# Kernel tuning notes

Measured on AMD Instinct MI355X. Metric: run time of the kernel, lower is better.

Reference implementation:

```python
import jax, jax.numpy as jnp
import numpy as np

HRNN = 2e-11  # seconds per step; t grid is in nanoseconds (x1e9), step = 0.02
W0, W1 = -20.0, 10.0          # fixed oscillator coupling weights
X0 = (0.4736, 0.8745, 1.8497)  # fixed initial state


def setup_inputs() -> dict:
    key = jax.random.key(0)
    ks = jax.random.split(key, 9)
    B, T, NIN, NHI, NHO, NOUT = 1024, 2048, 8, 64, 64, 1
    g = lambda k, shape, s: jax.random.normal(k, shape, jnp.float32) * s
    return {
        "inputdata": jax.random.normal(ks[0], (B, T, NIN), jnp.float32),
        "Wni": g(ks[1], (NHI, NIN), 1.0 / np.sqrt(NIN)),   # nonlinearinput
        "bni": g(ks[2], (NHI,), 0.1),
        "Wli": g(ks[3], (1, NHI), 1.0 / np.sqrt(NHI)),     # linearinput
        "bli": g(ks[4], (1,), 0.1),
        "tau": jnp.zeros((1,), jnp.float32),                # nn.Parameter(Tensor(1))
        "Wn": g(ks[5], (NHO, 3), 1.0 / np.sqrt(3.0)),      # nonlinear readout
        "bn": g(ks[6], (NHO,), 0.1),
        "Wl": g(ks[7], (NOUT, NHO), 1.0 / np.sqrt(NHO)),   # linear readout
        "bl": g(ks[8], (NOUT,), 0.1),
    }


def reference(inputdata, Wni, bni, Wli, bli, tau, Wn, bn, Wl, bl):
    B, T, NIN = inputdata.shape
    tg = jnp.linspace(0.0, HRNN * (T - 1) * 1e9, T).astype(jnp.float32)
    u = inputdata  # [B, T, NIN]
    x0 = jnp.broadcast_to(jnp.array(X0, jnp.float32)[None, :], (B, 3))

    def lin_interp(t):
        # clamp-to-edge linear interpolation of u along the time grid
        ind = jnp.clip(jnp.searchsorted(tg, t), 1, T - 1)
        t_lo, t_hi = tg[ind - 1], tg[ind]
        frac = jnp.clip((t - t_lo) / (t_hi - t_lo), 0.0, 1.0)
        u_lo = u[:, ind - 1, :]
        return u_lo + (u[:, ind, :] - u_lo) * frac  # [B, NIN]

    def f(t, x):
        ut = lin_interp(t)
        dparam = jax.nn.sigmoid(ut @ Wni.T + bni) @ Wli.T + bli  # [B, 1]
        tx = jnp.tanh(x)
        dx = jnp.stack(
            (-x[:, 0] + tx[:, 1],
             -x[:, 1] + tx[:, 2],
             -x[:, 2] + W0 * tx[:, 0] + W1 * tx[:, 1]),
            axis=1,
        )
        return dx / jnp.exp(tau + dparam)  # [B, 3]

    def step(x, ts):
        # torchdiffeq 'rk4' = fourth-order 3/8 rule between grid points
        t0, t1 = ts
        h = t1 - t0
        k1 = f(t0, x)
        k2 = f(t0 + h / 3, x + h * k1 / 3)
        k3 = f(t0 + 2 * h / 3, x + h * (k2 - k1 / 3))
        k4 = f(t1, x + h * (k1 - k2 + k3))
        xn = x + h * (k1 + 3 * k2 + 3 * k3 + k4) / 8
        return xn, xn

    _, xs = jax.lax.scan(step, x0, (tg[:-1], tg[1:]))  # [T-1, B, 3]
    outrnn = jnp.concatenate([x0[None], xs], axis=0).transpose(1, 0, 2)  # [B, T, 3]
    hid = jax.nn.sigmoid(outrnn @ Wn.T + bn)  # [B, T, NHO]
    return hid @ Wl.T + bl  # [B, T, NOUT]
```

## Files before the change

kernel.cpp:

```cpp
#include <hip/hip_runtime.h>

#define BB 1024
#define TT 2048
#define NIN 8
#define NHI 64

#define CS 2.8853900817779268f
#define NL2E 1.4426950408889634f
#define DELTA (40.94f / 2047.0f)

typedef float v2f __attribute__((ext_vector_type(2)));

__device__ __forceinline__ v2f vfma(v2f a, v2f b, v2f c) {
    return __builtin_elementwise_fma(a, b, c);
}

template<int CTRL>
__device__ __forceinline__ float qperm(float x) {
    int r = __builtin_amdgcn_mov_dpp(__float_as_int(x), CTRL, 0xF, 0xF, true);
    return __int_as_float(r);
}

__global__ __launch_bounds__(256) void precompute_r(
    const float* __restrict__ u, const float* __restrict__ Wni,
    const float* __restrict__ bni, const float* __restrict__ Wli,
    const float* __restrict__ bli, const float* __restrict__ tau,
    float* __restrict__ r3)
{
    int lt = threadIdx.x;
    int lane = lt & 63;
    int gw = blockIdx.x * 4 + (lt >> 6);
    int b = gw / 33;
    int chunk = gw % 33;
    int s = chunk * 63 + lane;
    int sc = s < TT ? s : TT - 1;
    int b2 = b + 512;

    const float4* upA = reinterpret_cast<const float4*>(u + ((long long)b  * TT + sc) * NIN);
    const float4* upB = reinterpret_cast<const float4*>(u + ((long long)b2 * TT + sc) * NIN);
    float4 A0 = upA[0], A1 = upA[1];
    float4 B0 = upB[0], B1 = upB[1];
    v2f u0 = {A0.x, B0.x}, u1 = {A0.y, B0.y}, u2 = {A0.z, B0.z}, u3 = {A0.w, B0.w};
    v2f u4 = {A1.x, B1.x}, u5 = {A1.y, B1.y}, u6 = {A1.z, B1.z}, u7 = {A1.w, B1.w};

    v2f d0 = {0.f, 0.f}, d1 = {0.f, 0.f}, d2 = {0.f, 0.f};
    #pragma unroll 8
    for (int j = 0; j < NHI; j++) {
        const float* wj = Wni + j * NIN;
        float bj = bni[j];
        v2f z = {bj, bj};
        z = vfma((v2f){wj[0], wj[0]}, u0, z);
        z = vfma((v2f){wj[1], wj[1]}, u1, z);
        z = vfma((v2f){wj[2], wj[2]}, u2, z);
        z = vfma((v2f){wj[3], wj[3]}, u3, z);
        z = vfma((v2f){wj[4], wj[4]}, u4, z);
        z = vfma((v2f){wj[5], wj[5]}, u5, z);
        z = vfma((v2f){wj[6], wj[6]}, u6, z);
        z = vfma((v2f){wj[7], wj[7]}, u7, z);
        v2f zn;
        zn.x = __shfl_down(z.x, 1);
        zn.y = __shfl_down(z.y, 1);
        v2f dz = zn - z;
        v2f zc  = z  * (v2f){-NL2E, -NL2E};
        v2f dzc = dz * (v2f){-NL2E / 3.0f, -NL2E / 3.0f};
        v2f e0, edz;
        e0.x  = __builtin_amdgcn_exp2f(zc.x);
        e0.y  = __builtin_amdgcn_exp2f(zc.y);
        edz.x = __builtin_amdgcn_exp2f(dzc.x);
        edz.y = __builtin_amdgcn_exp2f(dzc.y);
        v2f e1 = e0 * edz;
        v2f e2 = e1 * edz;
        v2f q0 = e0 + 1.0f, q1 = e1 + 1.0f, q2 = e2 + 1.0f;
        v2f P12 = q1 * q2;
        v2f Dn = q0 * P12;
        v2f rD;
        rD.x = __builtin_amdgcn_rcpf(Dn.x);
        rD.y = __builtin_amdgcn_rcpf(Dn.y);
        v2f P02 = q0 * q2;
        v2f P01 = q0 * q1;
        float wl = Wli[j];
        v2f wr = rD * (v2f){wl, wl};
        d0 = vfma(wr, P12, d0);
        d1 = vfma(wr, P02, d1);
        d2 = vfma(wr, P01, d2);
    }
    float base = tau[0] + bli[0];
    float g0a = DELTA * __builtin_amdgcn_exp2f((base + d0.x) * -NL2E);
    float g1a = DELTA * __builtin_amdgcn_exp2f((base + d1.x) * -NL2E);
    float g2a = DELTA * __builtin_amdgcn_exp2f((base + d2.x) * -NL2E);
    float g0b = DELTA * __builtin_amdgcn_exp2f((base + d0.y) * -NL2E);
    float g1b = DELTA * __builtin_amdgcn_exp2f((base + d1.y) * -NL2E);
    float g2b = DELTA * __builtin_amdgcn_exp2f((base + d2.y) * -NL2E);

    if (s < TT) {
        float* pA = r3 + ((long long)b  * TT + s) * 3;
        float* pB = r3 + ((long long)b2 * TT + s) * 3;
        pA[0] = g0a;
        pB[0] = g0b;
        if (lane < 63 && s < TT - 1) {
            pA[1] = g1a; pA[2] = g2a;
            pB[1] = g1b; pB[2] = g2b;
        }
    }
}

__global__ __launch_bounds__(64) void scan_kernel(
    const float* __restrict__ r3, float* __restrict__ xs)
{
    int gt = blockIdx.x * 64 + threadIdx.x;
    int b = gt >> 2;
    int l = gt & 3;

    const float4* rp = reinterpret_cast<const float4*>(r3 + (long long)b * TT * 3);
    int comp = (l == 3) ? 1 : l;
    float* xc = xs + (long long)comp * BB * TT + (long long)b * TT;

    bool is2 = (l == 2);
    float cA = is2 ? 40.0f * CS : -2.0f * CS;
    float cB = is2 ? -20.0f * CS : 0.0f;
    float Kl = is2 ? -10.0f * CS : CS;

    float X = (l == 0) ? 0.4736f * CS : (is2 ? 1.8497f * CS : 0.8745f * CS);

#define STEP(G1v, G2v, G3v, G4v) do { \
    float g1 = (G1v), g2 = (G2v), g3 = (G3v); \
    float q  = g1 * (1.0f / 3.0f); \
    float g4_8 = (G4v) * 0.125f; \
    float cA1 = q * cA,    cB1 = q * cB; \
    float cA2 = g2 * cA,   cB2 = g2 * cB; \
    float cA3 = g3 * cA,   cB3 = g3 * cB; \
    float cA4 = g4_8 * cA, cB4 = g4_8 * cB; \
     \
    float e1 = __builtin_amdgcn_exp2f(X); \
    float rho1 = __builtin_amdgcn_rcpf(1.0f + e1); \
    float KmX = Kl - X; \
    float pb2 = fmaf(q, KmX, X); \
    float p11 = qperm<0x89>(rho1), p21 = qperm<0x10>(rho1); \
    float S2 = fmaf(cA1, p11, fmaf(cB1, p21, pb2)); \
    float V1 = fmaf(cA, p11, cB * p21); \
    float W1 = V1 + KmX; \
     \
    float e2 = __builtin_amdgcn_exp2f(S2); \
    float rho2 = __builtin_amdgcn_rcpf(1.0f + e2); \
    float KmS2 = Kl - S2; \
    float pb3 = fmaf(g2, KmS2, fmaf(-q, W1, X)); \
    float p12 = qperm<0x89>(rho2), p22 = qperm<0x10>(rho2); \
    float S3 = fmaf(cA2, p12, fmaf(cB2, p22, pb3)); \
    float V2 = fmaf(cA, p12, cB * p22); \
    float W2 = V2 + KmS2; \
     \
    float e3 = __builtin_amdgcn_exp2f(S3); \
    float rho3 = __builtin_amdgcn_rcpf(1.0f + e3); \
    float KmS3 = Kl - S3; \
    float pb4 = fmaf(g3, KmS3, fmaf(-g2, W2, fmaf(g1, W1, X))); \
    float p13 = qperm<0x89>(rho3), p23 = qperm<0x10>(rho3); \
    float S4 = fmaf(cA3, p13, fmaf(cB3, p23, pb4)); \
    float V3 = fmaf(cA, p13, cB * p23); \
    float W3 = V3 + KmS3; \
     \
    float e4 = __builtin_amdgcn_exp2f(S4); \
    float rho4 = __builtin_amdgcn_rcpf(1.0f + e4); \
    float KmS4 = Kl - S4; \
    float t3 = fmaf(3.0f * g3, W3, fmaf(3.0f * g2, W2, g1 * W1)); \
    float pbX = fmaf(g4_8, KmS4, fmaf(0.125f, t3, X)); \
    float p14 = qperm<0x89>(rho4), p24 = qperm<0x10>(rho4); \
    X = fmaf(cA4, p14, fmaf(cB4, p24, pbX)); \
} while (0)

    float4 f0 = rp[0], f1 = rp[1], f2 = rp[2];
    float4 n0 = rp[3], n1 = rp[4], n2 = rp[5];

    for (int j = 0; j < 510; j++) {
        float4 m0 = rp[3 * j + 6], m1 = rp[3 * j + 7], m2 = rp[3 * j + 8];
        float4 ov;
        ov.x = X;
        STEP(f0.x, f0.y, f0.z, f0.w);  ov.y = X;
        STEP(f0.w, f1.x, f1.y, f1.z);  ov.z = X;
        STEP(f1.z, f1.w, f2.x, f2.y);  ov.w = X;
        *reinterpret_cast<float4*>(xc + 4 * j) = ov;
        STEP(f2.y, f2.z, f2.w, n0.x);
        f0 = n0; f1 = n1; f2 = n2;
        n0 = m0; n1 = m1; n2 = m2;
    }
    {
        float4 ov;
        ov.x = X;
        STEP(f0.x, f0.y, f0.z, f0.w);  ov.y = X;
        STEP(f0.w, f1.x, f1.y, f1.z);  ov.z = X;
        STEP(f1.z, f1.w, f2.x, f2.y);  ov.w = X;
        *reinterpret_cast<float4*>(xc + 4 * 510) = ov;
        STEP(f2.y, f2.z, f2.w, n0.x);
        f0 = n0; f1 = n1; f2 = n2;
    }
    {
        float4 ov;
        ov.x = X;
        STEP(f0.x, f0.y, f0.z, f0.w);  ov.y = X;
        STEP(f0.w, f1.x, f1.y, f1.z);  ov.z = X;
        STEP(f1.z, f1.w, f2.x, f2.y);  ov.w = X;
        *reinterpret_cast<float4*>(xc + 4 * 511) = ov;
    }
#undef STEP
}

__global__ __launch_bounds__(256) void out_kernel(
    const float* __restrict__ xs, const float* __restrict__ Wn,
    const float* __restrict__ bn, const float* __restrict__ Wl,
    const float* __restrict__ bl, float* __restrict__ out)
{
    const long long HALF = (long long)BB * TT / 2;
    int lt = threadIdx.x;
    long long tid = (long long)blockIdx.x * 256 + lt;
    long long tid2 = tid + HALF;

    v2f cs0 = { xs[tid],                        xs[tid2] };
    v2f cs1 = { xs[(long long)BB * TT + tid],   xs[(long long)BB * TT + tid2] };
    v2f cs2 = { xs[(long long)2 * BB * TT + tid], xs[(long long)2 * BB * TT + tid2] };
    cs0 = cs0 * -0.5f;
    cs1 = cs1 * -0.5f;
    cs2 = cs2 * -0.5f;

    v2f acc = {0.f, 0.f};
    #pragma unroll 8
    for (int j = 0; j < NHI; j++) {
        float w0 = Wn[3 * j], w1 = Wn[3 * j + 1], w2 = Wn[3 * j + 2];
        float bz = bn[j] * -NL2E;
        v2f z = vfma((v2f){w0, w0}, cs0,
                vfma((v2f){w1, w1}, cs1,
                vfma((v2f){w2, w2}, cs2, (v2f){bz, bz})));
        float ea = __builtin_amdgcn_exp2f(z.x);
        float eb = __builtin_amdgcn_exp2f(z.y);
        float qa = 1.0f + ea, qb = 1.0f + eb;
        float rD = __builtin_amdgcn_rcpf(qa * qb);
        float wr = Wl[j] * rD;
        v2f sw = {qb, qa};
        acc = vfma((v2f){wr, wr}, sw, acc);
    }
    out[tid]  = acc.x + bl[0];
    out[tid2] = acc.y + bl[0];
}

extern "C" void kernel_launch(void* const* d_in, const int* in_sizes, int n_in,
                              void* d_out, int out_size, void* d_ws, size_t ws_size,
                              hipStream_t stream) {
    const float* u    = (const float*)d_in[0];
    const float* Wni  = (const float*)d_in[1];
    const float* bni  = (const float*)d_in[2];
    const float* Wli  = (const float*)d_in[3];
    const float* bli  = (const float*)d_in[4];
    const float* tau  = (const float*)d_in[5];
    const float* Wn   = (const float*)d_in[6];
    const float* bn   = (const float*)d_in[7];
    const float* Wl   = (const float*)d_in[8];
    const float* bl   = (const float*)d_in[9];
    float* out = (float*)d_out;

    float* r3 = (float*)d_ws;
    float* xs = r3 + (size_t)3 * BB * TT;

    precompute_r<<<(512 * 33) / 4, 256, 0, stream>>>(u, Wni, bni, Wli, bli, tau, r3);
    scan_kernel<<<(BB * 4) / 64, 64, 0, stream>>>(r3, xs);
    out_kernel<<<(BB * TT / 2) / 256, 256, 0, stream>>>(xs, Wn, bn, Wl, bl, out);
}
```

Baseline: 397.4 us.

## Permute before reciprocal in scan step and batch four sigmoids per rcp

In the RK4 scan step, the DPP lane permutes now act on 1+exp before the reciprocal, with one rcp per permuted value. This moves the permute off the rcp→use dependency chain at the cost of an extra rcp per stage. The output kernel now handles four elements per thread and shares one reciprocal across four sigmoid denominators, which cuts transcendental ops but risks overflow from multiplying four denominators.

```diff
diff --git a/kernel.cpp b/kernel.cpp
--- a/kernel.cpp
+++ b/kernel.cpp
@@ -132,38 +132,46 @@
     float cA4 = g4_8 * cA, cB4 = g4_8 * cB; \
      \
     float e1 = __builtin_amdgcn_exp2f(X); \
-    float rho1 = __builtin_amdgcn_rcpf(1.0f + e1); \
+    float a1v = 1.0f + e1; \
+    float ap11 = qperm<0x89>(a1v), ap21 = qperm<0x10>(a1v); \
+    float p11 = __builtin_amdgcn_rcpf(ap11); \
+    float p21 = __builtin_amdgcn_rcpf(ap21); \
     float KmX = Kl - X; \
     float pb2 = fmaf(q, KmX, X); \
-    float p11 = qperm<0x89>(rho1), p21 = qperm<0x10>(rho1); \
     float S2 = fmaf(cA1, p11, fmaf(cB1, p21, pb2)); \
     float V1 = fmaf(cA, p11, cB * p21); \
     float W1 = V1 + KmX; \
      \
     float e2 = __builtin_amdgcn_exp2f(S2); \
-    float rho2 = __builtin_amdgcn_rcpf(1.0f + e2); \
+    float a2v = 1.0f + e2; \
+    float ap12 = qperm<0x89>(a2v), ap22 = qperm<0x10>(a2v); \
+    float p12 = __builtin_amdgcn_rcpf(ap12); \
+    float p22 = __builtin_amdgcn_rcpf(ap22); \
     float KmS2 = Kl - S2; \
     float pb3 = fmaf(g2, KmS2, fmaf(-q, W1, X)); \
-    float p12 = qperm<0x89>(rho2), p22 = qperm<0x10>(rho2); \
     float S3 = fmaf(cA2, p12, fmaf(cB2, p22, pb3)); \
     float V2 = fmaf(cA, p12, cB * p22); \
     float W2 = V2 + KmS2; \
      \
     float e3 = __builtin_amdgcn_exp2f(S3); \
-    float rho3 = __builtin_amdgcn_rcpf(1.0f + e3); \
+    float a3v = 1.0f + e3; \
+    float ap13 = qperm<0x89>(a3v), ap23 = qperm<0x10>(a3v); \
+    float p13 = __builtin_amdgcn_rcpf(ap13); \
+    float p23 = __builtin_amdgcn_rcpf(ap23); \
     float KmS3 = Kl - S3; \
     float pb4 = fmaf(g3, KmS3, fmaf(-g2, W2, fmaf(g1, W1, X))); \
-    float p13 = qperm<0x89>(rho3), p23 = qperm<0x10>(rho3); \
     float S4 = fmaf(cA3, p13, fmaf(cB3, p23, pb4)); \
     float V3 = fmaf(cA, p13, cB * p23); \
     float W3 = V3 + KmS3; \
      \
     float e4 = __builtin_amdgcn_exp2f(S4); \
-    float rho4 = __builtin_amdgcn_rcpf(1.0f + e4); \
+    float a4v = 1.0f + e4; \
+    float ap14 = qperm<0x89>(a4v), ap24 = qperm<0x10>(a4v); \
+    float p14 = __builtin_amdgcn_rcpf(ap14); \
+    float p24 = __builtin_amdgcn_rcpf(ap24); \
     float KmS4 = Kl - S4; \
     float t3 = fmaf(3.0f * g3, W3, fmaf(3.0f * g2, W2, g1 * W1)); \
     float pbX = fmaf(g4_8, KmS4, fmaf(0.125f, t3, X)); \
-    float p14 = qperm<0x89>(rho4), p24 = qperm<0x10>(rho4); \
     X = fmaf(cA4, p14, fmaf(cB4, p24, pbX)); \
 } while (0)
 
@@ -208,36 +216,50 @@
     const float* __restrict__ bn, const float* __restrict__ Wl,
     const float* __restrict__ bl, float* __restrict__ out)
 {
-    const long long HALF = (long long)BB * TT / 2;
+    const long long QT = (long long)BB * TT / 4;
     int lt = threadIdx.x;
     long long tid = (long long)blockIdx.x * 256 + lt;
-    long long tid2 = tid + HALF;
-
-    v2f cs0 = { xs[tid],                        xs[tid2] };
-    v2f cs1 = { xs[(long long)BB * TT + tid],   xs[(long long)BB * TT + tid2] };
-    v2f cs2 = { xs[(long long)2 * BB * TT + tid], xs[(long long)2 * BB * TT + tid2] };
-    cs0 = cs0 * -0.5f;
-    cs1 = cs1 * -0.5f;
-    cs2 = cs2 * -0.5f;
-
-    v2f acc = {0.f, 0.f};
+    long long t0 = tid, t1 = tid + QT, t2 = tid + 2 * QT, t3i = tid + 3 * QT;
+    const float* x1p = xs + (long long)BB * TT;
+    const float* x2p = xs + (long long)2 * BB * TT;
+
+    v2f csA0 = { xs[t0],  xs[t1]  }, csB0 = { xs[t2],  xs[t3i]  };
+    v2f csA1 = { x1p[t0], x1p[t1] }, csB1 = { x1p[t2], x1p[t3i] };
+    v2f csA2 = { x2p[t0], x2p[t1] }, csB2 = { x2p[t2], x2p[t3i] };
+    csA0 = csA0 * -0.5f;  csB0 = csB0 * -0.5f;
+    csA1 = csA1 * -0.5f;  csB1 = csB1 * -0.5f;
+    csA2 = csA2 * -0.5f;  csB2 = csB2 * -0.5f;
+
+    float acc0 = 0.f, acc1 = 0.f, acc2 = 0.f, acc3 = 0.f;
     #pragma unroll 8
     for (int j = 0; j < NHI; j++) {
         float w0 = Wn[3 * j], w1 = Wn[3 * j + 1], w2 = Wn[3 * j + 2];
         float bz = bn[j] * -NL2E;
-        v2f z = vfma((v2f){w0, w0}, cs0,
-                vfma((v2f){w1, w1}, cs1,
-                vfma((v2f){w2, w2}, cs2, (v2f){bz, bz})));
-        float ea = __builtin_amdgcn_exp2f(z.x);
-        float eb = __builtin_amdgcn_exp2f(z.y);
-        float qa = 1.0f + ea, qb = 1.0f + eb;
-        float rD = __builtin_amdgcn_rcpf(qa * qb);
-        float wr = Wl[j] * rD;
-        v2f sw = {qb, qa};
-        acc = vfma((v2f){wr, wr}, sw, acc);
-    }
-    out[tid]  = acc.x + bl[0];
-    out[tid2] = acc.y + bl[0];
+        v2f zA = vfma((v2f){w0, w0}, csA0,
+                 vfma((v2f){w1, w1}, csA1,
+                 vfma((v2f){w2, w2}, csA2, (v2f){bz, bz})));
+        v2f zB = vfma((v2f){w0, w0}, csB0,
+                 vfma((v2f){w1, w1}, csB1,
+                 vfma((v2f){w2, w2}, csB2, (v2f){bz, bz})));
+        float q0 = 1.0f + __builtin_amdgcn_exp2f(zA.x);
+        float q1 = 1.0f + __builtin_amdgcn_exp2f(zA.y);
+        float q2 = 1.0f + __builtin_amdgcn_exp2f(zB.x);
+        float q3 = 1.0f + __builtin_amdgcn_exp2f(zB.y);
+        float p01 = q0 * q1, p23 = q2 * q3;
+        float rD = __builtin_amdgcn_rcpf(p01 * p23);
+        float wl = Wl[j];
+        float w01 = wl * (p23 * rD);
+        float w23 = wl * (p01 * rD);
+        acc0 = fmaf(w01, q1, acc0);
+        acc1 = fmaf(w01, q0, acc1);
+        acc2 = fmaf(w23, q3, acc2);
+        acc3 = fmaf(w23, q2, acc3);
+    }
+    float blv = bl[0];
+    out[t0]  = acc0 + blv;
+    out[t1]  = acc1 + blv;
+    out[t2]  = acc2 + blv;
+    out[t3i] = acc3 + blv;
 }
 
 extern "C" void kernel_launch(void* const* d_in, const int* in_sizes, int n_in,
@@ -260,5 +282,5 @@
 
     precompute_r<<<(512 * 33) / 4, 256, 0, stream>>>(u, Wni, bni, Wli, bli, tau, r3);
     scan_kernel<<<(BB * 4) / 64, 64, 0, stream>>>(r3, xs);
-    out_kernel<<<(BB * TT / 2) / 256, 256, 0, stream>>>(xs, Wn, bn, Wl, bl, out);
-}
+    out_kernel<<<(BB * TT / 4) / 256, 256, 0, stream>>>(xs, Wn, bn, Wl, bl, out);
+}
```

Measured after the change: 397.7 us. No clear change (+0.1%).
